# Kernel tuning notes

Hardware: AMD Instinct MI355X
Metric: run time of the kernel (lower is better)

Reference implementation:

```python
import jax, jax.numpy as jnp
import numpy as np

B, S, D, H = 4, 2048, 1024, 16
HD = D // H


def setup_inputs() -> dict:
    key = jax.random.key(0)
    k1, k2, k3 = jax.random.split(key, 3)
    x = jax.random.normal(k1, (B, S, D), dtype=jnp.float32)
    w_qkv = jax.random.normal(k2, (D, 3 * D), dtype=jnp.float32) * (1.0 / np.sqrt(D))
    w_out = jax.random.normal(k3, (D, D), dtype=jnp.float32) * (1.0 / np.sqrt(D))
    return {"x": x, "w_qkv": w_qkv, "w_out": w_out}


def reference(x, w_qkv, w_out):
    bsz, seq_len, d = x.shape
    qkv = x @ w_qkv  # [B, S, 3D]
    q, k, v = jnp.split(qkv, 3, axis=-1)
    # [B, H, S, HD]
    q = q.reshape(bsz, seq_len, H, HD).transpose(0, 2, 1, 3)
    k = k.reshape(bsz, seq_len, H, HD).transpose(0, 2, 1, 3)
    v = v.reshape(bsz, seq_len, H, HD).transpose(0, 2, 1, 3)
    scale = 1.0 / np.sqrt(HD)
    scores = jnp.einsum('bhqd,bhkd->bhqk', q, k) * scale  # [B, H, S, S]
    causal = jnp.tril(jnp.ones((seq_len, seq_len), dtype=bool))
    scores = jnp.where(causal[None, None], scores, -jnp.inf)
    weights = jax.nn.softmax(scores, axis=-1)
    ctx = jnp.einsum('bhqk,bhkd->bhqd', weights, v)
    ctx = ctx.transpose(0, 2, 1, 3).reshape(bsz, seq_len, d)
    return ctx @ w_out
```

## Files before the change

kernel.cpp:

```cpp
#include <hip/hip_runtime.h>
#include <stdint.h>

typedef unsigned short u16;
typedef __attribute__((ext_vector_type(4))) float f32x4;
typedef __attribute__((ext_vector_type(8))) __bf16 bf16x8;
typedef __attribute__((ext_vector_type(8))) u16 u16x8;
typedef __attribute__((ext_vector_type(4))) u16 u16x4;
typedef __attribute__((ext_vector_type(2))) unsigned u32x2;

static constexpr int kB = 4, kS = 2048, kD = 1024, kH = 16, kHD = 64;
static constexpr int M1 = kB * kS;
static constexpr int N1 = 3 * kD;
static constexpr int K1 = kD;

#define SCLF 0.18033688011112042f
#define MFMA16(a, b, c) __builtin_amdgcn_mfma_f32_16x16x32_bf16((a), (b), (c), 0, 0, 0)

union U4 { unsigned u[4]; bf16x8 v; };

__device__ __forceinline__ u16 f2bf(float f) {
  union { float f; uint32_t u; } c; c.f = f;
  uint32_t u = c.u + 0x7FFFu + ((c.u >> 16) & 1u);
  return (u16)(u >> 16);
}

__device__ __forceinline__ unsigned pkbf(float a, float b) {
  union { __bf16 h[2]; unsigned u; } c;
  c.h[0] = (__bf16)a; c.h[1] = (__bf16)b;
  return c.u;
}

__device__ __forceinline__ float max3f(float a, float b, float c) {
  return fmaxf(fmaxf(a, b), c);
}

__device__ __forceinline__ void gload_lds16(const u16* g, u16* l) {
  __builtin_amdgcn_global_load_lds(
      (const __attribute__((address_space(1))) unsigned int*)g,
      (__attribute__((address_space(3))) unsigned int*)l, 16, 0, 0);
}

__global__ __launch_bounds__(256) void k_prep(const float* __restrict__ x,
                                              const float* __restrict__ w_qkv,
                                              const float* __restrict__ w_out,
                                              u16* __restrict__ x_bf,
                                              u16* __restrict__ wqkvT,
                                              u16* __restrict__ woutT) {
  const int bid = blockIdx.x;
  if (bid < 8192) {
    int i = (bid * 256 + threadIdx.x) * 4;
    f32x4 v = *(const f32x4*)(x + i);
    u16x4 r;
    r[0] = f2bf(v[0]); r[1] = f2bf(v[1]); r[2] = f2bf(v[2]); r[3] = f2bf(v[3]);
    *(u16x4*)(x_bf + i) = r;
    return;
  }
  __shared__ float t[32][33];
  const float* w; u16* wt; int N, idx;
  if (bid < 8192 + 3072) { idx = bid - 8192;  w = w_qkv; wt = wqkvT; N = N1; }
  else                   { idx = bid - 11264; w = w_out; wt = woutT; N = kD; }
  const int ntn = N >> 5;
  const int n0 = (idx % ntn) * 32, k0 = (idx / ntn) * 32;
  const int tx = threadIdx.x & 31, ty = threadIdx.x >> 5;
  for (int r = ty; r < 32; r += 8)
    t[r][tx] = w[(size_t)(k0 + r) * N + n0 + tx];
  __syncthreads();
  for (int r = ty; r < 32; r += 8)
    wt[(size_t)(n0 + r) * K1 + k0 + tx] = f2bf(t[tx][r]);
}

template <int MODE>
__global__ __launch_bounds__(512) void k_gemm_bt(const u16* __restrict__ A,
                                                 const u16* __restrict__ BT,
                                                 u16* __restrict__ obf,
                                                 float* __restrict__ of,
                                                 int M, int N, int K) {
  __shared__ __align__(16) u16 Asb[3][128 * 64];
  __shared__ __align__(16) u16 Bsb[3][256 * 64];

  const int tid = threadIdx.x;
  const int wave = tid >> 6, lane = tid & 63;
  const int l15 = lane & 15, l16 = lane >> 4;

  const int bid = blockIdx.x;
  const int qch = gridDim.x >> 3;
  const int swz = (bid & 7) * qch + (bid >> 3);
  const int ntN = N >> 8;
  const int row0 = (swz / ntN) * 128, col0 = (swz % ntN) * 256;
  const int wm = (wave >> 2) * 64, wn = (wave & 3) * 64;

  f32x4 acc[4][4];
#pragma unroll
  for (int i = 0; i < 4; ++i)
#pragma unroll
    for (int j = 0; j < 4; ++j) acc[i][j] = f32x4{0.f, 0.f, 0.f, 0.f};

  const int lr = lane >> 3, ls = lane & 7;
  const u16* srcA[2];
#pragma unroll
  for (int j = 0; j < 2; ++j) {
    const int r = (wave * 2 + j) * 8 + lr;
    srcA[j] = A + (size_t)(row0 + r) * K + (ls ^ (r & 7)) * 8;
  }
  const u16* srcB[4];
#pragma unroll
  for (int j = 0; j < 4; ++j) {
    const int r = (wave * 4 + j) * 8 + lr;
    srcB[j] = BT + (size_t)(col0 + r) * K + (ls ^ (r & 7)) * 8;
  }

  const int nT = K >> 6;

#define STAGE(t)                                                        \
  {                                                                     \
    const int buf_ = (t) % 3;                                           \
    const int kt_ = (t) * 64;                                           \
    _Pragma("unroll")                                                   \
    for (int j = 0; j < 2; ++j)                                         \
      gload_lds16(srcA[j] + kt_, &Asb[buf_][(wave * 2 + j) * 512]);     \
    _Pragma("unroll")                                                   \
    for (int j = 0; j < 4; ++j)                                         \
      gload_lds16(srcB[j] + kt_, &Bsb[buf_][(wave * 4 + j) * 512]);     \
  }

  STAGE(0);
  STAGE(1);
  asm volatile("s_waitcnt vmcnt(6)" ::: "memory");
  __builtin_amdgcn_s_barrier();

  for (int t = 0; t < nT; ++t) {
    const u16* As = &Asb[t % 3][0];
    const u16* Bs = &Bsb[t % 3][0];
    const bool pf = (t + 2 < nT);
    const int buf2 = (t + 2) % 3;
    const int kt2 = (t + 2) * 64;
    bf16x8 af[4], bfv[4];

#pragma unroll
    for (int f = 0; f < 4; ++f) {
      const int ra = wm + f * 16 + l15;
      af[f] = *(const bf16x8*)&As[ra * 64 + ((l16 ^ (ra & 7)) * 8)];
      const int rb = wn + f * 16 + l15;
      bfv[f] = *(const bf16x8*)&Bs[rb * 64 + ((l16 ^ (rb & 7)) * 8)];
    }
    if (pf) {
      gload_lds16(srcA[0] + kt2, &Asb[buf2][(wave * 2 + 0) * 512]);
      gload_lds16(srcA[1] + kt2, &Asb[buf2][(wave * 2 + 1) * 512]);
      gload_lds16(srcB[0] + kt2, &Bsb[buf2][(wave * 4 + 0) * 512]);
    }
    __builtin_amdgcn_sched_barrier(0);
    __builtin_amdgcn_s_barrier();
    asm volatile("s_waitcnt lgkmcnt(0)" ::: "memory");
    __builtin_amdgcn_sched_barrier(0);
    __builtin_amdgcn_s_setprio(1);
#pragma unroll
    for (int fm = 0; fm < 4; ++fm)
#pragma unroll
      for (int fn = 0; fn < 4; ++fn)
        acc[fm][fn] = MFMA16(af[fm], bfv[fn], acc[fm][fn]);
    __builtin_amdgcn_s_setprio(0);
    __builtin_amdgcn_sched_barrier(0);
    __builtin_amdgcn_s_barrier();

#pragma unroll
    for (int f = 0; f < 4; ++f) {
      const int ra = wm + f * 16 + l15;
      af[f] = *(const bf16x8*)&As[ra * 64 + (((4 + l16) ^ (ra & 7)) * 8)];
      const int rb = wn + f * 16 + l15;
      bfv[f] = *(const bf16x8*)&Bs[rb * 64 + (((4 + l16) ^ (rb & 7)) * 8)];
    }
    if (pf) {
      gload_lds16(srcB[1] + kt2, &Bsb[buf2][(wave * 4 + 1) * 512]);
      gload_lds16(srcB[2] + kt2, &Bsb[buf2][(wave * 4 + 2) * 512]);
      gload_lds16(srcB[3] + kt2, &Bsb[buf2][(wave * 4 + 3) * 512]);
    }
    if (pf)                asm volatile("s_waitcnt vmcnt(6)" ::: "memory");
    else if (t + 1 < nT)   asm volatile("s_waitcnt vmcnt(0)" ::: "memory");
    __builtin_amdgcn_sched_barrier(0);
    __builtin_amdgcn_s_barrier();
    asm volatile("s_waitcnt lgkmcnt(0)" ::: "memory");
    __builtin_amdgcn_sched_barrier(0);
    __builtin_amdgcn_s_setprio(1);
#pragma unroll
    for (int fm = 0; fm < 4; ++fm)
#pragma unroll
      for (int fn = 0; fn < 4; ++fn)
        acc[fm][fn] = MFMA16(af[fm], bfv[fn], acc[fm][fn]);
    __builtin_amdgcn_s_setprio(0);
    __builtin_amdgcn_sched_barrier(0);
    __builtin_amdgcn_s_barrier();
  }

#pragma unroll
  for (int fm = 0; fm < 4; ++fm)
#pragma unroll
    for (int fn = 0; fn < 4; ++fn) {
      const int n = col0 + wn + fn * 16 + l15;
#pragma unroll
      for (int j = 0; j < 4; ++j) {
        const int m = row0 + wm + fm * 16 + l16 * 4 + j;
        float v = acc[fm][fn][j];
        if constexpr (MODE == 0) {
          const int which = n >> 10, d = n & 1023;
          const int h = d >> 6, hd = d & 63;
          const int b = m >> 11, s = m & 2047;
          if (which == 0) v *= SCLF;
          obf[((((size_t)which * 4 + b) * 16 + h) * 2048 + s) * 64 + hd] = f2bf(v);
        } else {
          of[(size_t)m * N + n] = v;
        }
      }
    }
#undef STAGE
}

__global__ __launch_bounds__(512, 4) void k_attn(const u16* __restrict__ Qg,
                                                 const u16* __restrict__ Kg,
                                                 const u16* __restrict__ Vg,
                                                 u16* __restrict__ ctx) {
  __shared__ __align__(16) u16 Ks[2][64 * 64];
  __shared__ __align__(16) unsigned Vt[2][2048];
  __shared__ __align__(16) unsigned Pl[8 * 256];

  const int bid = blockIdx.x;
  const int xcd = bid & 7, i2 = bid >> 3;
  const int bh = xcd * 8 + (i2 & 7);
  const int p = i2 >> 3;
  const int bb = bh >> 4, hh = bh & 15;
  const int tid = threadIdx.x;
  const int wave = tid >> 6, lane = tid & 63;
  const int l15 = lane & 15, l16 = lane >> 4;

  const u16* Qb = Qg + (size_t)bh * kS * kHD;
  const u16* Kb = Kg + (size_t)bh * kS * kHD;
  const u16* Vb = Vg + (size_t)bh * kS * kHD;

  const int kkey = tid >> 3, ksl = tid & 7;
  const int do4 = tid & 15, kp = tid >> 4;
  unsigned* Pw = Pl + wave * 256 + l15 * 16;
  const int pm = ((l15 >> 1) & 3) << 2;

  U4 onesu;
#pragma unroll
  for (int i = 0; i < 4; ++i) onesu.u[i] = 0x3F803F80u;
  const bf16x8 vones = onesu.v;

  unsigned voff[4];
#pragma unroll
  for (int i = 0; i < 4; ++i) {
    const int d = do4 * 4 + i;
    voff[i] = d * 32 + (kp ^ ((((d & 7) ^ (d >> 3))) << 2));
  }
  const u16* ksrc = Kb + (size_t)kkey * 64 + (ksl ^ (kkey & 7)) * 8;

  for (int phase = 0; phase < 2; ++phase) {
    const int qsup = phase ? (15 - p) : p;
    const int qstart = qsup * 128 + wave * 16;
    const int ntiles = 2 * qsup + 2;

    bf16x8 bq[2];
#pragma unroll
    for (int ds = 0; ds < 2; ++ds)
      bq[ds] = *(const bf16x8*)(Qb + (size_t)(qstart + l15) * 64 + ds * 32 + l16 * 8);

    f32x4 acc[4];
#pragma unroll
    for (int i = 0; i < 4; ++i) acc[i] = f32x4{0.f, 0.f, 0.f, 0.f};
    f32x4 acc_l = f32x4{0.f, 0.f, 0.f, 0.f};
    float mrow = -3e38f;

    __syncthreads();

    u16x4 va, vb;
    {
      const u16* vs = Vb + (size_t)(2 * kp) * 64 + do4 * 4;
      va = *(const u16x4*)vs; vb = *(const u16x4*)(vs + 64);
    }
#pragma unroll
    for (int i = 0; i < 4; ++i)
      Vt[0][voff[i]] = (unsigned)va[i] | ((unsigned)vb[i] << 16);
    {
      const u16* vs = Vb + (size_t)(64 + 2 * kp) * 64 + do4 * 4;
      va = *(const u16x4*)vs; vb = *(const u16x4*)(vs + 64);
    }
    gload_lds16(ksrc, &Ks[0][wave * 512]);

    for (int t = 0; t < ntiles; ++t) {
      const int kv0 = t * 64;
      __syncthreads();

      if (t + 1 < ntiles) {
        const int nb = (t + 1) & 1;
#pragma unroll
        for (int i = 0; i < 4; ++i)
          Vt[nb][voff[i]] = (unsigned)va[i] | ((unsigned)vb[i] << 16);
        gload_lds16(ksrc + (size_t)(t + 1) * 64 * 64, &Ks[nb][wave * 512]);
        if (t + 2 < ntiles) {
          const u16* vs = Vb + (size_t)((t + 2) * 64 + 2 * kp) * 64 + do4 * 4;
          va = *(const u16x4*)vs; vb = *(const u16x4*)(vs + 64);
        }
      }

      if (kv0 > qstart + 15) continue;

      const u16* Ksb = &Ks[t & 1][0];
      const unsigned* Vtb = &Vt[t & 1][0];
      const int qv = qstart + l15;
      const bool have1 = (kv0 + 32 <= qstart + 15);

      f32x4 stA0 = f32x4{0.f, 0.f, 0.f, 0.f}, stA1 = stA0;
      f32x4 stB0 = stA0, stB1 = stA0;
      __builtin_amdgcn_s_setprio(1);
#pragma unroll
      for (int ds = 0; ds < 2; ++ds) {
        const int slot = ((ds * 4 + l16) ^ (l15 & 7)) * 8;
        bf16x8 ak0 = *(const bf16x8*)&Ksb[(l15) * 64 + slot];
        stA0 = MFMA16(ak0, bq[ds], stA0);
        bf16x8 ak1 = *(const bf16x8*)&Ksb[(16 + l15) * 64 + slot];
        stA1 = MFMA16(ak1, bq[ds], stA1);
        if (have1) {
          bf16x8 bk0 = *(const bf16x8*)&Ksb[(32 + l15) * 64 + slot];
          stB0 = MFMA16(bk0, bq[ds], stB0);
          bf16x8 bk1 = *(const bf16x8*)&Ksb[(48 + l15) * 64 + slot];
          stB1 = MFMA16(bk1, bq[ds], stB1);
        }
      }
      __builtin_amdgcn_s_setprio(0);

      if (kv0 + 31 > qstart) {
#pragma unroll
        for (int j = 0; j < 4; ++j) {
          const int key = kv0 + l16 * 4 + j;
          stA0[j] = (key <= qv) ? stA0[j] : -3e38f;
          stA1[j] = (key + 16 <= qv) ? stA1[j] : -3e38f;
        }
      }
      if (have1 && (kv0 + 63 > qstart)) {
#pragma unroll
        for (int j = 0; j < 4; ++j) {
          const int key = kv0 + 32 + l16 * 4 + j;
          stB0[j] = (key <= qv) ? stB0[j] : -3e38f;
          stB1[j] = (key + 16 <= qv) ? stB1[j] : -3e38f;
        }
      }

      float tl;
      {
        const float mA = fmaxf(max3f(stA0[0], stA0[1], stA0[2]),
                               max3f(stA0[3], stA1[0], stA1[1]));
        tl = max3f(stA1[2], stA1[3], mA);
        if (have1) {
          const float mB = fmaxf(max3f(stB0[0], stB0[1], stB0[2]),
                                 max3f(stB0[3], stB1[0], stB1[1]));
          tl = fmaxf(tl, max3f(stB1[2], stB1[3], mB));
        }
      }

      float mn;
      if (__all(tl <= mrow + 8.0f)) {
        mn = mrow;
      } else {
        float tj = fmaxf(tl, __shfl_xor(tl, 16, 64));
        tj = fmaxf(tj, __shfl_xor(tj, 32, 64));
        mn = fmaxf(mrow, tj);
        const float al = exp2f(mrow - mn);
        mrow = mn;
        acc_l[0] *= al;
#pragma unroll
        for (int i = 0; i < 4; ++i)
#pragma unroll
          for (int j = 0; j < 4; ++j) acc[i][j] *= al;
      }

      {
#pragma unroll
        for (int j = 0; j < 4; ++j) {
          stA0[j] = exp2f(stA0[j] - mn);
          stA1[j] = exp2f(stA1[j] - mn);
        }
        const unsigned p0 = pkbf(stA0[0], stA0[1]);
        const unsigned p1 = pkbf(stA0[2], stA0[3]);
        const unsigned p2 = pkbf(stA1[0], stA1[1]);
        const unsigned p3 = pkbf(stA1[2], stA1[3]);
        *(u32x2*)&Pw[(l16 * 2) ^ pm] = u32x2{p0, p1};
        *(u32x2*)&Pw[(8 + l16 * 2) ^ pm] = u32x2{p2, p3};
        U4 f;
        f = *(const U4*)&Pw[(l16 * 4) ^ pm];
        __builtin_amdgcn_s_setprio(1);
        acc_l = MFMA16(vones, f.v, acc_l);
#pragma unroll
        for (int dg = 0; dg < 4; ++dg) {
          const int d = dg * 16 + l15;
          const int addr = d * 32 + ((l16 * 4) ^ ((((d & 7) ^ (d >> 3))) << 2));
          const bf16x8 vf = *(const bf16x8*)&Vtb[addr];
          acc[dg] = MFMA16(vf, f.v, acc[dg]);
        }
        __builtin_amdgcn_s_setprio(0);
      }
      if (have1) {
#pragma unroll
        for (int j = 0; j < 4; ++j) {
          stB0[j] = exp2f(stB0[j] - mn);
          stB1[j] = exp2f(stB1[j] - mn);
        }
        const unsigned p0 = pkbf(stB0[0], stB0[1]);
        const unsigned p1 = pkbf(stB0[2], stB0[3]);
        const unsigned p2 = pkbf(stB1[0], stB1[1]);
        const unsigned p3 = pkbf(stB1[2], stB1[3]);
        *(u32x2*)&Pw[(l16 * 2) ^ pm] = u32x2{p0, p1};
        *(u32x2*)&Pw[(8 + l16 * 2) ^ pm] = u32x2{p2, p3};
        U4 f;
        f = *(const U4*)&Pw[(l16 * 4) ^ pm];
        __builtin_amdgcn_s_setprio(1);
        acc_l = MFMA16(vones, f.v, acc_l);
#pragma unroll
        for (int dg = 0; dg < 4; ++dg) {
          const int d = dg * 16 + l15;
          const int addr = d * 32 + ((16 + l16 * 4) ^ ((((d & 7) ^ (d >> 3))) << 2));
          const bf16x8 vf = *(const bf16x8*)&Vtb[addr];
          acc[dg] = MFMA16(vf, f.v, acc[dg]);
        }
        __builtin_amdgcn_s_setprio(0);
      }
    }

    const float rl = 1.0f / acc_l[0];
    u16* orow = ctx + ((size_t)bb * kS + (qstart + l15)) * kD + hh * 64;
#pragma unroll
    for (int dg = 0; dg < 4; ++dg) {
      u16x4 pk;
#pragma unroll
      for (int j = 0; j < 4; ++j) pk[j] = f2bf(acc[dg][j] * rl);
      *(u16x4*)&orow[dg * 16 + l16 * 4] = pk;
    }
  }
}

extern "C" void kernel_launch(void* const* d_in, const int* in_sizes, int n_in,
                              void* d_out, int out_size, void* d_ws, size_t ws_size,
                              hipStream_t stream) {
  const float* x     = (const float*)d_in[0];
  const float* w_qkv = (const float*)d_in[1];
  const float* w_out = (const float*)d_in[2];
  float* out = (float*)d_out;

  u16* ws    = (u16*)d_ws;
  u16* x_bf  = ws;
  u16* wqkvT = x_bf + (size_t)M1 * K1;
  u16* woutT = wqkvT + (size_t)N1 * K1;
  u16* qkv   = woutT + (size_t)kD * kD;
  u16* ctx   = qkv + (size_t)3 * kB * kH * kS * kHD;

  k_prep<<<dim3(12288), 256, 0, stream>>>(x, w_qkv, w_out, x_bf, wqkvT, woutT);

  k_gemm_bt<0><<<dim3(768), 512, 0, stream>>>(x_bf, wqkvT, qkv, nullptr,
                                              M1, N1, K1);

  const u16* Qg = qkv;
  const u16* Kg = qkv + (size_t)kB * kH * kS * kHD;
  const u16* Vg = qkv + (size_t)2 * kB * kH * kS * kHD;
  k_attn<<<dim3(512), 512, 0, stream>>>(Qg, Kg, Vg, ctx);

  k_gemm_bt<1><<<dim3(256), 512, 0, stream>>>(ctx, woutT, nullptr, out,
                                              M1, kD, K1);
}
```

Baseline: 181.6 us.

## Write V pre-transposed from QKV GEMM epilogue and DMA it directly in attention

```diff
diff --git a/kernel.cpp b/kernel.cpp
--- a/kernel.cpp
+++ b/kernel.cpp
@@ -111,22 +111,22 @@
 
   const int nT = K >> 6;
 
-#define STAGE(t)                                                        \
-  {                                                                     \
-    const int buf_ = (t) % 3;                                           \
-    const int kt_ = (t) * 64;                                           \
-    _Pragma("unroll")                                                   \
-    for (int j = 0; j < 2; ++j)                                         \
-      gload_lds16(srcA[j] + kt_, &Asb[buf_][(wave * 2 + j) * 512]);     \
-    _Pragma("unroll")                                                   \
-    for (int j = 0; j < 4; ++j)                                         \
-      gload_lds16(srcB[j] + kt_, &Bsb[buf_][(wave * 4 + j) * 512]);     \
-  }
-
-  STAGE(0);
-  STAGE(1);
-  asm volatile("s_waitcnt vmcnt(6)" ::: "memory");
-  __builtin_amdgcn_s_barrier();
+  {
+#pragma unroll
+    for (int j = 0; j < 2; ++j)
+      gload_lds16(srcA[j], &Asb[0][(wave * 2 + j) * 512]);
+#pragma unroll
+    for (int j = 0; j < 4; ++j)
+      gload_lds16(srcB[j], &Bsb[0][(wave * 4 + j) * 512]);
+#pragma unroll
+    for (int j = 0; j < 2; ++j)
+      gload_lds16(srcA[j] + 64, &Asb[1][(wave * 2 + j) * 512]);
+#pragma unroll
+    for (int j = 0; j < 4; ++j)
+      gload_lds16(srcB[j] + 64, &Bsb[1][(wave * 4 + j) * 512]);
+    asm volatile("s_waitcnt vmcnt(6)" ::: "memory");
+    __builtin_amdgcn_s_barrier();
+  }
 
   for (int t = 0; t < nT; ++t) {
     const u16* As = &Asb[t % 3][0];
@@ -189,6 +189,32 @@
     __builtin_amdgcn_s_setprio(0);
     __builtin_amdgcn_sched_barrier(0);
     __builtin_amdgcn_s_barrier();
+  }
+
+  if (MODE == 0 && col0 >= 2048) {
+    u16* T = &Bsb[0][0];
+#pragma unroll
+    for (int fm = 0; fm < 4; ++fm)
+#pragma unroll
+      for (int fn = 0; fn < 4; ++fn) {
+        const int nl = wn + fn * 16 + l15;
+#pragma unroll
+        for (int j = 0; j < 4; ++j) {
+          const int ml = wm + fm * 16 + l16 * 4 + j;
+          T[nl * 128 + ml] = f2bf(acc[fm][fn][j]);
+        }
+      }
+    __syncthreads();
+    const int r = tid >> 1, hb = (tid & 1) * 64;
+    const int d = (col0 + r) & 1023;
+    const int b = row0 >> 11, s0 = row0 & 2047;
+    u16* dst = obf + ((((size_t)8 + b) * 16 + (d >> 6)) * 64 + (d & 63)) * 2048 +
+               s0 + hb;
+    const u16* srcT = &T[r * 128 + hb];
+#pragma unroll
+    for (int i = 0; i < 8; ++i)
+      *(u16x8*)(dst + i * 8) = *(const u16x8*)(srcT + i * 8);
+    return;
   }
 
 #pragma unroll
@@ -211,7 +237,6 @@
         }
       }
     }
-#undef STAGE
 }
 
 __global__ __launch_bounds__(512, 4) void k_attn(const u16* __restrict__ Qg,
@@ -219,7 +244,7 @@
                                                  const u16* __restrict__ Vg,
                                                  u16* __restrict__ ctx) {
   __shared__ __align__(16) u16 Ks[2][64 * 64];
-  __shared__ __align__(16) unsigned Vt[2][2048];
+  __shared__ __align__(16) u16 Vs[2][64 * 64];
   __shared__ __align__(16) unsigned Pl[8 * 256];
 
   const int bid = blockIdx.x;
@@ -236,7 +261,6 @@
   const u16* Vb = Vg + (size_t)bh * kS * kHD;
 
   const int kkey = tid >> 3, ksl = tid & 7;
-  const int do4 = tid & 15, kp = tid >> 4;
   unsigned* Pw = Pl + wave * 256 + l15 * 16;
   const int pm = ((l15 >> 1) & 3) << 2;
 
@@ -245,13 +269,8 @@
   for (int i = 0; i < 4; ++i) onesu.u[i] = 0x3F803F80u;
   const bf16x8 vones = onesu.v;
 
-  unsigned voff[4];
-#pragma unroll
-  for (int i = 0; i < 4; ++i) {
-    const int d = do4 * 4 + i;
-    voff[i] = d * 32 + (kp ^ ((((d & 7) ^ (d >> 3))) << 2));
-  }
   const u16* ksrc = Kb + (size_t)kkey * 64 + (ksl ^ (kkey & 7)) * 8;
+  const u16* vsrc = Vb + (size_t)kkey * 2048 + (ksl ^ (kkey & 7)) * 8;
 
   for (int phase = 0; phase < 2; ++phase) {
     const int qsup = phase ? (15 - p) : p;
@@ -271,19 +290,8 @@
 
     __syncthreads();
 
-    u16x4 va, vb;
-    {
-      const u16* vs = Vb + (size_t)(2 * kp) * 64 + do4 * 4;
-      va = *(const u16x4*)vs; vb = *(const u16x4*)(vs + 64);
-    }
-#pragma unroll
-    for (int i = 0; i < 4; ++i)
-      Vt[0][voff[i]] = (unsigned)va[i] | ((unsigned)vb[i] << 16);
-    {
-      const u16* vs = Vb + (size_t)(64 + 2 * kp) * 64 + do4 * 4;
-      va = *(const u16x4*)vs; vb = *(const u16x4*)(vs + 64);
-    }
     gload_lds16(ksrc, &Ks[0][wave * 512]);
+    gload_lds16(vsrc, &Vs[0][wave * 512]);
 
     for (int t = 0; t < ntiles; ++t) {
       const int kv0 = t * 64;
@@ -291,20 +299,14 @@
 
       if (t + 1 < ntiles) {
         const int nb = (t + 1) & 1;
-#pragma unroll
-        for (int i = 0; i < 4; ++i)
-          Vt[nb][voff[i]] = (unsigned)va[i] | ((unsigned)vb[i] << 16);
-        gload_lds16(ksrc + (size_t)(t + 1) * 64 * 64, &Ks[nb][wave * 512]);
-        if (t + 2 < ntiles) {
-          const u16* vs = Vb + (size_t)((t + 2) * 64 + 2 * kp) * 64 + do4 * 4;
-          va = *(const u16x4*)vs; vb = *(const u16x4*)(vs + 64);
-        }
+        gload_lds16(ksrc + (size_t)(t + 1) * 4096, &Ks[nb][wave * 512]);
+        gload_lds16(vsrc + (size_t)(t + 1) * 64, &Vs[nb][wave * 512]);
       }
 
       if (kv0 > qstart + 15) continue;
 
       const u16* Ksb = &Ks[t & 1][0];
-      const unsigned* Vtb = &Vt[t & 1][0];
+      const u16* Vtb = &Vs[t & 1][0];
       const int qv = qstart + l15;
       const bool have1 = (kv0 + 32 <= qstart + 15);
 
@@ -391,8 +393,8 @@
 #pragma unroll
         for (int dg = 0; dg < 4; ++dg) {
           const int d = dg * 16 + l15;
-          const int addr = d * 32 + ((l16 * 4) ^ ((((d & 7) ^ (d >> 3))) << 2));
-          const bf16x8 vf = *(const bf16x8*)&Vtb[addr];
+          const bf16x8 vf =
+              *(const bf16x8*)&Vtb[d * 64 + ((l16 ^ (d & 7)) * 8)];
           acc[dg] = MFMA16(vf, f.v, acc[dg]);
         }
         __builtin_amdgcn_s_setprio(0);
@@ -416,8 +418,8 @@
 #pragma unroll
         for (int dg = 0; dg < 4; ++dg) {
           const int d = dg * 16 + l15;
-          const int addr = d * 32 + ((16 + l16 * 4) ^ ((((d & 7) ^ (d >> 3))) << 2));
-          const bf16x8 vf = *(const bf16x8*)&Vtb[addr];
+          const bf16x8 vf =
+              *(const bf16x8*)&Vtb[d * 64 + (((4 + l16) ^ (d & 7)) * 8)];
           acc[dg] = MFMA16(vf, f.v, acc[dg]);
         }
         __builtin_amdgcn_s_setprio(0);
```

New measurement: 183.0 us. Within noise of the previous version (+0.7%).
